# Kernel optimization log

Hardware: AMD Instinct MI355X
Metric: run time of the kernel (lower is better)

## Reference

```python
import jax, jax.numpy as jnp
import numpy as np
from jax import lax

EPS = 1e-5
WBITS, BBITS, ABITS = 8, 8, 11  # weight/bias/activation precisions (class defaults)


def _ste_round(x):
    # straight-through estimator round (matches HAWQ-style fake quant)
    return x + lax.stop_gradient(jnp.round(x) - x)


def _quant_weight(w, bits):
    # symmetric per-output-channel weight quantization
    n = 2.0 ** (bits - 1) - 1.0
    s = lax.stop_gradient(jnp.max(jnp.abs(w.reshape(w.shape[0], -1)), axis=1)) / n
    s = jnp.maximum(s, 1e-8)
    w_int = jnp.clip(_ste_round(w / s[:, None, None, None]), -n - 1.0, n)
    return w_int, s


def _conv(x, w, stride, pad):
    return lax.conv_general_dilated(
        x, w, (stride, stride), ((pad, pad), (pad, pad)),
        dimension_numbers=('NCHW', 'OIHW', 'NCHW'))


def _quant_bn_conv(x, act_scale, w, gamma, beta, mean, var, stride, pad):
    # fold BN into conv (QuantBnConv2d), quantize folded weight per channel,
    # integer conv in the x/act_scale domain, rescale back to float
    f = gamma * lax.rsqrt(var + EPS)
    w_f = w * f[:, None, None, None]
    b_f = beta - mean * f
    w_int, w_s = _quant_weight(w_f, WBITS)
    nb = 2.0 ** (BBITS - 1) - 1.0
    b_s = w_s * act_scale  # [O]
    b_int = jnp.clip(_ste_round(b_f / b_s), -nb - 1.0, nb)
    x_int = x / act_scale
    y_int = _conv(x_int, w_int, stride, pad) + b_int[None, :, None, None]
    return y_int * b_s[None, :, None, None], w_s


def _quant_conv(x, act_scale, w, stride, pad):
    # plain QuantConv2d (shortcut path, no bias)
    w_int, w_s = _quant_weight(w, WBITS)
    y_int = _conv(x / act_scale, w_int, stride, pad)
    scale = w_s * act_scale  # [O]
    return y_int * scale[None, :, None, None], w_s


def _quant_act(x, bits):
    # QuantAct: symmetric dynamic requantization to `bits` bits
    n = 2.0 ** (bits - 1) - 1.0
    s = jnp.maximum(lax.stop_gradient(jnp.max(jnp.abs(x))) / n, 1e-8)
    xq = jnp.clip(_ste_round(x / s), -n - 1.0, n) * s
    return xq, s


def setup_inputs() -> dict:
    key = jax.random.key(0)
    ks = jax.random.split(key, 12)
    B, Cin, Cout, H = 64, 128, 256, 56
    return {
        'x': jax.random.normal(ks[0], (B, Cin, H, H), jnp.float32),
        'act_scale': jnp.ones((1,), jnp.float32) * 0.05,
        'w_sc': jax.random.normal(ks[1], (Cout, Cin, 1, 1), jnp.float32) * 0.05,
        'w1': jax.random.normal(ks[2], (Cout, Cin, 3, 3), jnp.float32) * 0.05,
        'g1': jax.random.uniform(ks[3], (Cout,), jnp.float32) + 0.5,
        'b1': jax.random.normal(ks[4], (Cout,), jnp.float32) * 0.1,
        'm1': jax.random.normal(ks[5], (Cout,), jnp.float32) * 0.1,
        'v1': jax.random.uniform(ks[6], (Cout,), jnp.float32) + 0.5,
        'w2': jax.random.normal(ks[7], (Cout, Cout, 3, 3), jnp.float32) * 0.05,
        'g2': jax.random.uniform(ks[8], (Cout,), jnp.float32) + 0.5,
        'b2': jax.random.normal(ks[9], (Cout,), jnp.float32) * 0.1,
        'm2': jax.random.normal(ks[10], (Cout,), jnp.float32) * 0.1,
        'v2': jax.random.uniform(ks[11], (Cout,), jnp.float32) + 0.5,
    }


def reference(x, act_scale, w_sc, w1, g1, b1, m1, v1, w2, g2, b2, m2, v2):
    # resize_identity branch of QBlock.forward (stride-2 stage transition)
    short_x, _ = _quant_conv(x, act_scale, w_sc, stride=2, pad=0)
    out, _ = _quant_bn_conv(x, act_scale, w1, g1, b1, m1, v1, stride=2, pad=1)
    out = jax.nn.relu(out)
    out, a = _quant_act(out, ABITS)
    out, _ = _quant_bn_conv(out, a, w2, g2, b2, m2, v2, stride=1, pad=1)
    out = jax.nn.relu(out)
    out, a = _quant_act(out, ABITS)
    out = jax.nn.relu(out + short_x)
    out, a = _quant_act(out, ABITS)
    return out, a
```

## Files before the change

kernel.cpp:

```cpp
#include <hip/hip_runtime.h>
#include <cstdio>
#include <cstdint>

typedef _Float16 h8 __attribute__((ext_vector_type(8)));
typedef _Float16 h4 __attribute__((ext_vector_type(4)));
typedef _Float16 h2 __attribute__((ext_vector_type(2)));
typedef float f4 __attribute__((ext_vector_type(4)));

#define GLD16(g, l) __builtin_amdgcn_global_load_lds( \
    (const __attribute__((address_space(1))) void*)(g), \
    (__attribute__((address_space(3))) void*)(l), 16, 0, 0)

static constexpr int HOUT = 28;
static constexpr long long NSP = 64LL * HOUT * HOUT;
static constexpr long long NEL = NSP * 256;
static constexpr int NSLOT = 64;
static constexpr int SLOTSTRIDE = 32;

__global__ void init_ws(int* __restrict__ slots, _Float16* __restrict__ zp)
{
    const int t = threadIdx.x;
    for (int i = t; i < 3 * NSLOT * SLOTSTRIDE; i += 256) slots[i] = 0;
    for (int i = t; i < 512; i += 256) zp[i] = (_Float16)0.f;
}

__device__ __forceinline__ float slot_max(const int* __restrict__ slots)
{
    float m = 0.f;
#pragma unroll
    for (int i = 0; i < NSLOT; ++i) m = fmaxf(m, __int_as_float(slots[i * SLOTSTRIDE]));
    return m;
}

__global__ void prep_w1(const float* __restrict__ w1, const float* __restrict__ g1,
                        const float* __restrict__ b1, const float* __restrict__ m1,
                        const float* __restrict__ v1, const float* __restrict__ asp,
                        _Float16* __restrict__ wq, float* __restrict__ scale1,
                        float* __restrict__ bias1)
{
    const int o = blockIdx.x, t = threadIdx.x;
    const float f = g1[o] * rsqrtf(v1[o] + 1e-5f);
    const float* wr = w1 + (size_t)o * 1152;
    float amax = 0.f;
    for (int i = t; i < 1152; i += 256) amax = fmaxf(amax, fabsf(wr[i] * f));
    __shared__ float red[256];
    red[t] = amax; __syncthreads();
    for (int s = 128; s > 0; s >>= 1) { if (t < s) red[t] = fmaxf(red[t], red[t + s]); __syncthreads(); }
    const float ws = fmaxf(red[0] / 127.f, 1e-8f);
    for (int idx = t; idx < 2304; idx += 256) {
        int p = idx >> 8, cc = idx & 255, ci = cc & 127;
        float q = fminf(fmaxf(rintf(wr[ci * 9 + p] * f / ws), -128.f), 127.f);
        wq[(size_t)o * 2304 + idx] = (_Float16)q;
    }
    if (t == 0) {
        const float bs = ws * asp[0];
        const float bf = b1[o] - m1[o] * f;
        float bq = fminf(fmaxf(rintf(bf / bs), -128.f), 127.f);
        scale1[o] = bs;
        bias1[o] = bq * bs;
    }
}

__global__ void prep_w2(const float* __restrict__ w2, const float* __restrict__ g2,
                        const float* __restrict__ b2, const float* __restrict__ m2,
                        const float* __restrict__ v2,
                        _Float16* __restrict__ wq, float* __restrict__ ws2,
                        float* __restrict__ b2f)
{
    const int o = blockIdx.x, t = threadIdx.x;
    const float f = g2[o] * rsqrtf(v2[o] + 1e-5f);
    const float* wr = w2 + (size_t)o * 2304;
    float amax = 0.f;
    for (int i = t; i < 2304; i += 256) amax = fmaxf(amax, fabsf(wr[i] * f));
    __shared__ float red[256];
    red[t] = amax; __syncthreads();
    for (int s = 128; s > 0; s >>= 1) { if (t < s) red[t] = fmaxf(red[t], red[t + s]); __syncthreads(); }
    const float ws = fmaxf(red[0] / 127.f, 1e-8f);
    for (int idx = t; idx < 2304; idx += 256) {
        int p = idx >> 8, ci = idx & 255;
        float q = fminf(fmaxf(rintf(wr[ci * 9 + p] * f / ws), -128.f), 127.f);
        wq[(size_t)o * 2304 + idx] = (_Float16)q;
    }
    if (t == 0) { ws2[o] = ws; b2f[o] = b2[o] - m2[o] * f; }
}

__global__ void prep_wsc(const float* __restrict__ wsc, const float* __restrict__ asp,
                         _Float16* __restrict__ wq, float* __restrict__ scale_sc)
{
    const int o = blockIdx.x, t = threadIdx.x;
    const float* wr = wsc + (size_t)o * 128;
    float amax = (t < 128) ? fabsf(wr[t]) : 0.f;
    __shared__ float red[256];
    red[t] = amax; __syncthreads();
    for (int s = 128; s > 0; s >>= 1) { if (t < s) red[t] = fmaxf(red[t], red[t + s]); __syncthreads(); }
    const float ws = fmaxf(red[0] / 127.f, 1e-8f);
    float q = fminf(fmaxf(rintf(wr[t & 127] / ws), -128.f), 127.f);
    wq[(size_t)o * 256 + t] = (_Float16)q;
    if (t == 0) scale_sc[o] = ws * asp[0];
}

__global__ void prep_x(const float* __restrict__ x, const float* __restrict__ asp,
                       _Float16* __restrict__ xf)
{
    const int b = blockIdx.x / 56, h = blockIdx.x - (blockIdx.x / 56) * 56;
    const float as = asp[0];
    __shared__ float tile[56 * 129];
    const float* src = x + ((size_t)b * 128 * 56 + h) * 56;
    for (int i = threadIdx.x; i < 7168; i += 256) {
        int c = i / 56, ww = i - c * 56;
        tile[ww * 129 + c] = src[(size_t)c * 3136 + ww] / as;
    }
    __syncthreads();
    _Float16* dst = xf + (size_t)(b * 56 + h) * 2 * 28 * 256;
    for (int j = threadIdx.x; j < 7168; j += 256) {
        int ww = j >> 7, q = j & 127;
        int cc = q * 2;
        int c0 = cc & 127, c1 = (cc + 1) & 127;
        float x0 = tile[ww * 129 + c0];
        float x1 = tile[ww * 129 + c1];
        h2 o;
        if (cc < 128) { o[0] = (_Float16)x0; o[1] = (_Float16)x1; }
        else {
            _Float16 h0 = (_Float16)x0, h1 = (_Float16)x1;
            o[0] = (_Float16)(x0 - (float)h0);
            o[1] = (_Float16)(x1 - (float)h1);
        }
        size_t eo = ((size_t)(ww & 1) * 28 + (ww >> 1)) * 256 + (size_t)cc;
        *(h2*)&dst[eo] = o;
    }
}

template<int MODE>
__global__ __launch_bounds__(512, 1)
void conv_k(const _Float16* __restrict__ Xf,
            const _Float16* __restrict__ Wq,
            const _Float16* __restrict__ Wsc,
            const float* __restrict__ scale,
            const float* __restrict__ bias,
            const float* __restrict__ scale_sc,
            float* __restrict__ Y,
            float* __restrict__ Ysc,
            int* __restrict__ slots,
            const _Float16* __restrict__ zp)
{
    constexpr int KT = 2304;
    constexpr int NSTEP = 72;
    __shared__ __attribute__((aligned(16))) _Float16 L[49152];
    __shared__ float wred[8];

    const int t = threadIdx.x;
    const int wave = t >> 6, lane = t & 63;
    const int wm = wave >> 2;
    const int wn = wave & 3;
    const int fr = lane & 15, fq = lane >> 4;

    const int orig = blockIdx.x;
    const int xcd = orig & 7, i8 = orig >> 3;
    const int wgid = (xcd < 4 ? xcd * 25 : 100 + (xcd - 4) * 24) + i8;
    const int n0 = wgid << 8;

    const int srow = wn * 64 + lane;
    const char* aSrc = (const char*)Wq + (size_t)srow * (KT * 2);
    const int nb = n0 + srow;
    const int bb = nb / 784;
    const int rbp = nb - bb * 784;
    const int ohb = rbp / 28, owb = rbp - (rbp / 28) * 28;

    const char* bptr = (const char*)zp;
    auto stage = [&](int tt, int slot) {
        char* base = (char*)L + slot * 32768;
        if ((tt & 7) == 0) {
            const int p = tt >> 3;
            const int kh = p / 3, kw = p - kh * 3;
            if constexpr (MODE == 0) {
                int ih = ohb * 2 - 1 + kh;
                int par = (kw == 1) ? 0 : 1;
                int j = (kw == 0) ? owb - 1 : owb;
                bool ok = ((unsigned)ih < 56u) && ((unsigned)j < 28u);
                bptr = ok ? (const char*)Xf + (((((size_t)bb * 56 + ih) * 2 + par) * 28 + j) << 9)
                          : (const char*)zp;
            } else {
                int ih = ohb - 1 + kh, iw = owb - 1 + kw;
                bool ok = ((unsigned)ih < 28u) && ((unsigned)iw < 28u);
                bptr = ok ? (const char*)Xf + ((((size_t)bb * 28 + ih) * 28 + iw) << 9)
                          : (const char*)zp;
            }
        }
        const size_t ka = (size_t)tt * 64;
        const int ko = (tt & 7) * 64;
        GLD16(aSrc + ka + wm * 16,          base + wm * 4096 + wn * 1024);
        GLD16(aSrc + ka + (2 + wm) * 16,    base + (2 + wm) * 4096 + wn * 1024);
        GLD16(bptr + ko + wm * 16,          base + 16384 + wm * 4096 + wn * 1024);
        GLD16(bptr + ko + (2 + wm) * 16,    base + 16384 + (2 + wm) * 4096 + wn * 1024);
    };

    f4 acc[8][4];
#pragma unroll
    for (int i = 0; i < 8; ++i)
#pragma unroll
        for (int j = 0; j < 4; ++j) acc[i][j] = f4{0.f, 0.f, 0.f, 0.f};

    stage(0, 0);
    stage(1, 1);
    int cs = 0, ns = 2;
#pragma unroll 1
    for (int it = 0; it < NSTEP - 1; ++it) {
        asm volatile("s_waitcnt vmcnt(4)" ::: "memory");
        __builtin_amdgcn_s_barrier();
        const _Float16* Sa = &L[cs * 16384];
        const _Float16* Sb = Sa + 8192;
        h8 af0[4], af1[4], bf[4];
#pragma unroll
        for (int i = 0; i < 4; ++i) {
            af0[i] = *(const h8*)&Sa[fq * 2048 + (wm * 128 + i * 16 + fr) * 8];
            bf[i]  = *(const h8*)&Sb[fq * 2048 + (wn * 64 + i * 16 + fr) * 8];
        }
#pragma unroll
        for (int i = 0; i < 4; ++i)
            af1[i] = *(const h8*)&Sa[fq * 2048 + (wm * 128 + 64 + i * 16 + fr) * 8];
        if (it + 2 < NSTEP) stage(it + 2, ns);
        __builtin_amdgcn_s_setprio(1);
#pragma unroll
        for (int mi = 0; mi < 4; ++mi)
#pragma unroll
            for (int ni = 0; ni < 4; ++ni)
                acc[mi][ni] = __builtin_amdgcn_mfma_f32_16x16x32_f16(af0[mi], bf[ni], acc[mi][ni], 0, 0, 0);
#pragma unroll
        for (int mi = 0; mi < 4; ++mi)
#pragma unroll
            for (int ni = 0; ni < 4; ++ni)
                acc[4 + mi][ni] = __builtin_amdgcn_mfma_f32_16x16x32_f16(af1[mi], bf[ni], acc[4 + mi][ni], 0, 0, 0);
        __builtin_amdgcn_s_setprio(0);
        cs = (cs == 2) ? 0 : cs + 1;
        ns = (ns == 2) ? 0 : ns + 1;
    }
    {
        asm volatile("s_waitcnt vmcnt(0)" ::: "memory");
        __builtin_amdgcn_s_barrier();
        const _Float16* Sa = &L[cs * 16384];
        const _Float16* Sb = Sa + 8192;
        h8 af0[4], af1[4], bf[4];
#pragma unroll
        for (int i = 0; i < 4; ++i) {
            af0[i] = *(const h8*)&Sa[fq * 2048 + (wm * 128 + i * 16 + fr) * 8];
            bf[i]  = *(const h8*)&Sb[fq * 2048 + (wn * 64 + i * 16 + fr) * 8];
        }
#pragma unroll
        for (int i = 0; i < 4; ++i)
            af1[i] = *(const h8*)&Sa[fq * 2048 + (wm * 128 + 64 + i * 16 + fr) * 8];
#pragma unroll
        for (int mi = 0; mi < 4; ++mi)
#pragma unroll
            for (int ni = 0; ni < 4; ++ni)
                acc[mi][ni] = __builtin_amdgcn_mfma_f32_16x16x32_f16(af0[mi], bf[ni], acc[mi][ni], 0, 0, 0);
#pragma unroll
        for (int mi = 0; mi < 4; ++mi)
#pragma unroll
            for (int ni = 0; ni < 4; ++ni)
                acc[4 + mi][ni] = __builtin_amdgcn_mfma_f32_16x16x32_f16(af1[mi], bf[ni], acc[4 + mi][ni], 0, 0, 0);
    }

    float tmax = 0.f;
#pragma unroll
    for (int mi = 0; mi < 8; ++mi) {
        const int m = wm * 128 + mi * 16 + fq * 4;
        const f4 sc = *(const f4*)&scale[m];
        const f4 bi = *(const f4*)&bias[m];
#pragma unroll
        for (int ni = 0; ni < 4; ++ni) {
            const int n = n0 + wn * 64 + ni * 16 + fr;
            f4 v = acc[mi][ni] * sc + bi;
            f4 r;
            r.x = fmaxf(v.x, 0.f); r.y = fmaxf(v.y, 0.f);
            r.z = fmaxf(v.z, 0.f); r.w = fmaxf(v.w, 0.f);
            tmax = fmaxf(tmax, fmaxf(fmaxf(r.x, r.y), fmaxf(r.z, r.w)));
            *(f4*)&Y[(size_t)n * 256 + m] = r;
        }
    }
#pragma unroll
    for (int off = 32; off > 0; off >>= 1)
        tmax = fmaxf(tmax, __shfl_xor(tmax, off));
    if (lane == 0) wred[wave] = tmax;
    __syncthreads();
    if (t == 0) {
        float mx = 0.f;
#pragma unroll
        for (int i = 0; i < 8; ++i) mx = fmaxf(mx, wred[i]);
        atomicMax(&slots[(wgid & (NSLOT - 1)) * SLOTSTRIDE], __float_as_int(mx));
    }

    if constexpr (MODE == 0) {
        const char* pb[4];
#pragma unroll
        for (int ni = 0; ni < 4; ++ni) {
            int n = n0 + wn * 64 + ni * 16 + fr;
            int b2 = n / 784;
            int r2 = n - b2 * 784;
            int oh2 = r2 / 28, ow2 = r2 - (r2 / 28) * 28;
            pb[ni] = (const char*)Xf + (((((size_t)b2 * 56 + oh2 * 2) * 2 + 0) * 28 + ow2) << 9);
        }
#pragma unroll
        for (int i = 0; i < 8; ++i)
#pragma unroll
            for (int j = 0; j < 4; ++j) acc[i][j] = f4{0.f, 0.f, 0.f, 0.f};
#pragma unroll 1
        for (int st = 0; st < 8; ++st) {
            h8 sf[8], bg[4];
#pragma unroll
            for (int mi = 0; mi < 8; ++mi)
                sf[mi] = *(const h8*)((const char*)Wsc +
                         (size_t)(wm * 128 + mi * 16 + fr) * 512 + st * 64 + fq * 16);
#pragma unroll
            for (int ni = 0; ni < 4; ++ni)
                bg[ni] = *(const h8*)(pb[ni] + st * 64 + fq * 16);
#pragma unroll
            for (int mi = 0; mi < 8; ++mi)
#pragma unroll
                for (int ni = 0; ni < 4; ++ni)
                    acc[mi][ni] = __builtin_amdgcn_mfma_f32_16x16x32_f16(sf[mi], bg[ni], acc[mi][ni], 0, 0, 0);
        }
#pragma unroll
        for (int mi = 0; mi < 8; ++mi) {
            const int m = wm * 128 + mi * 16 + fq * 4;
            const f4 ssc = *(const f4*)&scale_sc[m];
#pragma unroll
            for (int ni = 0; ni < 4; ++ni) {
                const int n = n0 + wn * 64 + ni * 16 + fr;
                f4 s = acc[mi][ni] * ssc;
                *(f4*)&Ysc[(size_t)n * 256 + m] = s;
            }
        }
    }
}

__global__ void mid_k(const int* __restrict__ slotsA, const float* __restrict__ ws2,
                      const float* __restrict__ b2f, float* __restrict__ scale2,
                      float* __restrict__ bias2, float* __restrict__ a1p)
{
    const int o = threadIdx.x;
    const float a1 = fmaxf(slot_max(slotsA) / 1023.f, 1e-8f);
    const float s2 = ws2[o] * a1;
    float bq = fminf(fmaxf(rintf(b2f[o] / s2), -128.f), 127.f);
    scale2[o] = s2;
    bias2[o] = bq * s2;
    if (o == 0) a1p[0] = a1;
}

__global__ void quant_x2(const float* __restrict__ t1, const float* __restrict__ a1p,
                         _Float16* __restrict__ x2)
{
    const size_t i = (size_t)blockIdx.x * 256 + threadIdx.x;
    const float a1 = a1p[0];
    f4 v = ((const f4*)t1)[i];
    h4 o;
    o[0] = (_Float16)fminf(rintf(v.x / a1), 1023.f);
    o[1] = (_Float16)fminf(rintf(v.y / a1), 1023.f);
    o[2] = (_Float16)fminf(rintf(v.z / a1), 1023.f);
    o[3] = (_Float16)fminf(rintf(v.w / a1), 1023.f);
    ((h4*)x2)[i] = o;
}

__global__ void add_short_k(const float* __restrict__ t2, const float* __restrict__ sh,
                            const int* __restrict__ slotsB, int* __restrict__ slotsC,
                            float* __restrict__ o3)
{
    const float a2 = fmaxf(slot_max(slotsB) / 1023.f, 1e-8f);
    const float inv_a2 = 1.f / a2;
    float tmax = 0.f;
    const size_t base = (size_t)blockIdx.x * 256 + threadIdx.x;
#pragma unroll
    for (int it = 0; it < 4; ++it) {
        const size_t i = base + (size_t)it * 802816;
        f4 v = ((const f4*)t2)[i];
        f4 s = ((const f4*)sh)[i];
        f4 r;
        r.x = fmaxf(fminf(rintf(v.x * inv_a2), 1023.f) * a2 + s.x, 0.f);
        r.y = fmaxf(fminf(rintf(v.y * inv_a2), 1023.f) * a2 + s.y, 0.f);
        r.z = fmaxf(fminf(rintf(v.z * inv_a2), 1023.f) * a2 + s.z, 0.f);
        r.w = fmaxf(fminf(rintf(v.w * inv_a2), 1023.f) * a2 + s.w, 0.f);
        ((f4*)o3)[i] = r;
        tmax = fmaxf(tmax, fmaxf(fmaxf(r.x, r.y), fmaxf(r.z, r.w)));
    }
#pragma unroll
    for (int off = 32; off > 0; off >>= 1)
        tmax = fmaxf(tmax, __shfl_xor(tmax, off));
    __shared__ float wred[4];
    if ((threadIdx.x & 63) == 0) wred[threadIdx.x >> 6] = tmax;
    __syncthreads();
    if (threadIdx.x == 0) {
        float mx = fmaxf(fmaxf(wred[0], wred[1]), fmaxf(wred[2], wred[3]));
        atomicMax(&slotsC[(blockIdx.x & (NSLOT - 1)) * SLOTSTRIDE], __float_as_int(mx));
    }
}

__global__ void finalize_k(const float* __restrict__ o3, const int* __restrict__ slotsC,
                           float* __restrict__ dout, int out_size)
{
    const int b = blockIdx.x / 28, oh = blockIdx.x - (blockIdx.x / 28) * 28;
    const float a3 = fmaxf(slot_max(slotsC) / 1023.f, 1e-8f);
    __shared__ float tile[28 * 257];
    const float* src = o3 + (size_t)(b * 28 + oh) * 28 * 256;
    for (int i = threadIdx.x; i < 7168; i += 256)
        tile[(i >> 8) * 257 + (i & 255)] = src[i];
    __syncthreads();
    for (int j = threadIdx.x; j < 7168; j += 256) {
        int c = j / 28, ww = j - (j / 28) * 28;
        float v = tile[ww * 257 + c];
        float q = fminf(rintf(v / a3), 1023.f);
        dout[(((size_t)b * 256 + c) * 28 + oh) * 28 + ww] = q * a3;
    }
    if (blockIdx.x == 0 && threadIdx.x == 0) dout[(size_t)out_size - 1] = a3;
}

extern "C" void kernel_launch(void* const* d_in, const int* in_sizes, int n_in,
                              void* d_out, int out_size, void* d_ws, size_t ws_size,
                              hipStream_t stream)
{
    const float* x   = (const float*)d_in[0];
    const float* as_ = (const float*)d_in[1];
    const float* wsc = (const float*)d_in[2];
    const float* w1  = (const float*)d_in[3];
    const float* g1  = (const float*)d_in[4];
    const float* b1  = (const float*)d_in[5];
    const float* m1  = (const float*)d_in[6];
    const float* v1  = (const float*)d_in[7];
    const float* w2  = (const float*)d_in[8];
    const float* g2  = (const float*)d_in[9];
    const float* b2  = (const float*)d_in[10];
    const float* m2  = (const float*)d_in[11];
    const float* v2  = (const float*)d_in[12];
    float* out = (float*)d_out;

    char* w = (char*)d_ws;
    size_t off = 0;
    auto alloc = [&](size_t bytes) { size_t c = off; off += (bytes + 255) & ~(size_t)255; return c; };
    const size_t oXF = alloc((size_t)64 * 56 * 56 * 256 * 2);
    const size_t oY1 = alloc((size_t)NEL * 4);
    const size_t oSH = alloc((size_t)NEL * 4);
    const size_t oX2 = alloc((size_t)NEL * 2);
    const size_t oW1 = alloc((size_t)256 * 2304 * 2);
    const size_t oW2 = alloc((size_t)256 * 2304 * 2);
    const size_t oWS = alloc((size_t)256 * 256 * 2);
    const size_t oSC = alloc((size_t)8 * 256 * 4);
    const size_t oMS = alloc(3 * NSLOT * SLOTSTRIDE * 4 + 2048);
    if (off > ws_size) {
        fprintf(stderr, "kernel_launch: ws too small: need %zu have %zu\n", off, ws_size);
        return;
    }

    _Float16* xf   = (_Float16*)(w + oXF);
    float*    y1   = (float*)(w + oY1);
    float*    sh   = (float*)(w + oSH);
    _Float16* x2   = (_Float16*)(w + oX2);
    _Float16* wq1  = (_Float16*)(w + oW1);
    _Float16* wq2  = (_Float16*)(w + oW2);
    _Float16* wscd = (_Float16*)(w + oWS);
    float* scl = (float*)(w + oSC);
    float *scale1 = scl, *bias1 = scl + 256, *scale_sc = scl + 512, *ws2 = scl + 768,
          *b2f = scl + 1024, *scale2 = scl + 1280, *bias2 = scl + 1536, *a1p = scl + 1792;
    int* slots  = (int*)(w + oMS);
    int* slotsA = slots;
    int* slotsB = slots + NSLOT * SLOTSTRIDE;
    int* slotsC = slots + 2 * NSLOT * SLOTSTRIDE;
    _Float16* zp = (_Float16*)(w + oMS + 3 * NSLOT * SLOTSTRIDE * 4);
    float* y2 = (float*)(w + oXF);
    float* o3 = (float*)(w + oY1);

    init_ws<<<1, 256, 0, stream>>>(slots, zp);
    prep_wsc<<<256, 256, 0, stream>>>(wsc, as_, wscd, scale_sc);
    prep_w1<<<256, 256, 0, stream>>>(w1, g1, b1, m1, v1, as_, wq1, scale1, bias1);
    prep_w2<<<256, 256, 0, stream>>>(w2, g2, b2, m2, v2, wq2, ws2, b2f);
    prep_x<<<64 * 56, 256, 0, stream>>>(x, as_, xf);
    conv_k<0><<<196, 512, 0, stream>>>(xf, wq1, wscd, scale1, bias1, scale_sc,
                                       y1, sh, slotsA, zp);
    mid_k<<<1, 256, 0, stream>>>(slotsA, ws2, b2f, scale2, bias2, a1p);
    quant_x2<<<12544, 256, 0, stream>>>(y1, a1p, x2);
    conv_k<1><<<196, 512, 0, stream>>>(x2, wq2, nullptr, scale2, bias2, nullptr,
                                       y2, nullptr, slotsB, zp);
    add_short_k<<<3136, 256, 0, stream>>>(y2, sh, slotsB, slotsC, o3);
    finalize_k<<<64 * 28, 256, 0, stream>>>(o3, slotsC, out, out_size);
}
```

Measured before the change: 366.4 us.

## Deepen conv main-loop pipeline to four LDS stages with split half-phases

Restructures the conv GEMM main loop from a 3-slot LDS ring to a 4-slot ring with a prefetch distance of 3 K-steps. Each K-step is split into two halves: each half issues half of the next stage's global-to-LDS loads, then runs 16 MFMAs, with barriers, lgkmcnt waits and sched_barriers between the halves. This is meant to keep more global loads in flight and interleave loads with MFMA work to hide memory latency. In exchange it uses more LDS (128KB), adds more barriers per iteration, and waits on vmcnt counts that depend on how many K-steps remain.

```diff
diff --git a/kernel.cpp b/kernel.cpp
--- a/kernel.cpp
+++ b/kernel.cpp
@@ -143,127 +143,118 @@
             int* __restrict__ slots,
             const _Float16* __restrict__ zp)
 {
-    constexpr int KT = 2304;
-    constexpr int NSTEP = 72;
-    __shared__ __attribute__((aligned(16))) _Float16 L[49152];
+    constexpr int NH = 72;
+    __shared__ __attribute__((aligned(16))) _Float16 L[65536];
     __shared__ float wred[8];
 
     const int t = threadIdx.x;
-    const int wave = t >> 6, lane = t & 63;
-    const int wm = wave >> 2;
-    const int wn = wave & 3;
-    const int fr = lane & 15, fq = lane >> 4;
+    const int w = t >> 6, lane = t & 63;
+    const int wm = w >> 2, wn = w & 3;
+    const int fr = lane & 15, fqr = lane >> 4;
 
     const int orig = blockIdx.x;
     const int xcd = orig & 7, i8 = orig >> 3;
     const int wgid = (xcd < 4 ? xcd * 25 : 100 + (xcd - 4) * 24) + i8;
     const int n0 = wgid << 8;
 
-    const int srow = wn * 64 + lane;
-    const char* aSrc = (const char*)Wq + (size_t)srow * (KT * 2);
+    const int srow = (w & 3) * 64 + lane;
+    const char* aSrc = (const char*)Wq + (size_t)srow * 4608;
     const int nb = n0 + srow;
     const int bb = nb / 784;
     const int rbp = nb - bb * 784;
     const int ohb = rbp / 28, owb = rbp - (rbp / 28) * 28;
+    const int fqs = w >> 2;
+    const int dgr = w * 64;
 
     const char* bptr = (const char*)zp;
-    auto stage = [&](int tt, int slot) {
-        char* base = (char*)L + slot * 32768;
-        if ((tt & 7) == 0) {
-            const int p = tt >> 3;
-            const int kh = p / 3, kw = p - kh * 3;
-            if constexpr (MODE == 0) {
-                int ih = ohb * 2 - 1 + kh;
-                int par = (kw == 1) ? 0 : 1;
-                int j = (kw == 0) ? owb - 1 : owb;
-                bool ok = ((unsigned)ih < 56u) && ((unsigned)j < 28u);
-                bptr = ok ? (const char*)Xf + (((((size_t)bb * 56 + ih) * 2 + par) * 28 + j) << 9)
-                          : (const char*)zp;
-            } else {
-                int ih = ohb - 1 + kh, iw = owb - 1 + kw;
-                bool ok = ((unsigned)ih < 28u) && ((unsigned)iw < 28u);
-                bptr = ok ? (const char*)Xf + ((((size_t)bb * 28 + ih) * 28 + iw) << 9)
-                          : (const char*)zp;
-            }
-        }
-        const size_t ka = (size_t)tt * 64;
-        const int ko = (tt & 7) * 64;
-        GLD16(aSrc + ka + wm * 16,          base + wm * 4096 + wn * 1024);
-        GLD16(aSrc + ka + (2 + wm) * 16,    base + (2 + wm) * 4096 + wn * 1024);
-        GLD16(bptr + ko + wm * 16,          base + 16384 + wm * 4096 + wn * 1024);
-        GLD16(bptr + ko + (2 + wm) * 16,    base + 16384 + (2 + wm) * 4096 + wn * 1024);
+    auto set_tap = [&](int kt) {
+        const int p = kt >> 3;
+        const int kh = p / 3, kw = p - kh * 3;
+        if constexpr (MODE == 0) {
+            int ih = ohb * 2 - 1 + kh;
+            int par = (kw == 1) ? 0 : 1;
+            int j = (kw == 0) ? owb - 1 : owb;
+            bool ok = ((unsigned)ih < 56u) && ((unsigned)j < 28u);
+            bptr = ok ? (const char*)Xf + (((((size_t)bb * 56 + ih) * 2 + par) * 28 + j) << 9)
+                      : (const char*)zp;
+        } else {
+            int ih = ohb - 1 + kh, iw = owb - 1 + kw;
+            bool ok = ((unsigned)ih < 28u) && ((unsigned)iw < 28u);
+            bptr = ok ? (const char*)Xf + ((((size_t)bb * 28 + ih) * 28 + iw) << 9)
+                      : (const char*)zp;
+        }
     };
 
+    auto stage_part = [&](int kt, int j) {
+        if (kt >= NH) return;
+        char* base = (char*)L + (size_t)(kt & 3) * 32768;
+        const int fq = 2 * j + fqs;
+        if (j == 0 && (kt & 7) == 0) set_tap(kt);
+        GLD16(aSrc + (size_t)kt * 64 + fq * 16, base + (j * 512 + dgr) * 16);
+        GLD16(bptr + (kt & 7) * 64 + fq * 16,   base + 16384 + (j * 512 + dgr) * 16);
+    };
+
     f4 acc[8][4];
 #pragma unroll
     for (int i = 0; i < 8; ++i)
 #pragma unroll
         for (int j = 0; j < 4; ++j) acc[i][j] = f4{0.f, 0.f, 0.f, 0.f};
 
-    stage(0, 0);
-    stage(1, 1);
-    int cs = 0, ns = 2;
+    stage_part(0, 0); stage_part(0, 1);
+    stage_part(1, 0); stage_part(1, 1);
+    stage_part(2, 0); stage_part(2, 1);
+    asm volatile("s_waitcnt vmcnt(8)" ::: "memory");
+    __builtin_amdgcn_s_barrier();
+
 #pragma unroll 1
-    for (int it = 0; it < NSTEP - 1; ++it) {
-        asm volatile("s_waitcnt vmcnt(4)" ::: "memory");
+    for (int kt = 0; kt < NH; ++kt) {
+        const char* SA = (const char*)L + (size_t)(kt & 3) * 32768;
+        const char* SB = SA + 16384;
+        h8 af0[4], bf[4];
+#pragma unroll
+        for (int i = 0; i < 4; ++i) {
+            af0[i] = *(const h8*)(SA + fqr * 4096 + (wm * 128 + i * 16 + fr) * 16);
+            bf[i]  = *(const h8*)(SB + fqr * 4096 + (wn * 64 + i * 16 + fr) * 16);
+        }
+        stage_part(kt + 3, 0);
         __builtin_amdgcn_s_barrier();
-        const _Float16* Sa = &L[cs * 16384];
-        const _Float16* Sb = Sa + 8192;
-        h8 af0[4], af1[4], bf[4];
-#pragma unroll
-        for (int i = 0; i < 4; ++i) {
-            af0[i] = *(const h8*)&Sa[fq * 2048 + (wm * 128 + i * 16 + fr) * 8];
-            bf[i]  = *(const h8*)&Sb[fq * 2048 + (wn * 64 + i * 16 + fr) * 8];
-        }
-#pragma unroll
-        for (int i = 0; i < 4; ++i)
-            af1[i] = *(const h8*)&Sa[fq * 2048 + (wm * 128 + 64 + i * 16 + fr) * 8];
-        if (it + 2 < NSTEP) stage(it + 2, ns);
+        asm volatile("s_waitcnt lgkmcnt(0)" ::: "memory");
+        __builtin_amdgcn_sched_barrier(0);
         __builtin_amdgcn_s_setprio(1);
 #pragma unroll
         for (int mi = 0; mi < 4; ++mi)
 #pragma unroll
             for (int ni = 0; ni < 4; ++ni)
                 acc[mi][ni] = __builtin_amdgcn_mfma_f32_16x16x32_f16(af0[mi], bf[ni], acc[mi][ni], 0, 0, 0);
+        __builtin_amdgcn_s_setprio(0);
+        __builtin_amdgcn_s_barrier();
+
+        h8 af1[4];
+#pragma unroll
+        for (int i = 0; i < 4; ++i)
+            af1[i] = *(const h8*)(SA + fqr * 4096 + (wm * 128 + 64 + i * 16 + fr) * 16);
+        stage_part(kt + 3, 1);
+        __builtin_amdgcn_s_barrier();
+        asm volatile("s_waitcnt lgkmcnt(0)" ::: "memory");
+        __builtin_amdgcn_sched_barrier(0);
+        __builtin_amdgcn_s_setprio(1);
 #pragma unroll
         for (int mi = 0; mi < 4; ++mi)
 #pragma unroll
             for (int ni = 0; ni < 4; ++ni)
                 acc[4 + mi][ni] = __builtin_amdgcn_mfma_f32_16x16x32_f16(af1[mi], bf[ni], acc[4 + mi][ni], 0, 0, 0);
         __builtin_amdgcn_s_setprio(0);
-        cs = (cs == 2) ? 0 : cs + 1;
-        ns = (ns == 2) ? 0 : ns + 1;
-    }
-    {
-        asm volatile("s_waitcnt vmcnt(0)" ::: "memory");
+        const int rem = (NH - 2) - kt;
+        if (rem >= 2)      { asm volatile("s_waitcnt vmcnt(8)" ::: "memory"); }
+        else if (rem == 1) { asm volatile("s_waitcnt vmcnt(4)" ::: "memory"); }
+        else if (rem == 0) { asm volatile("s_waitcnt vmcnt(0)" ::: "memory"); }
         __builtin_amdgcn_s_barrier();
-        const _Float16* Sa = &L[cs * 16384];
-        const _Float16* Sb = Sa + 8192;
-        h8 af0[4], af1[4], bf[4];
-#pragma unroll
-        for (int i = 0; i < 4; ++i) {
-            af0[i] = *(const h8*)&Sa[fq * 2048 + (wm * 128 + i * 16 + fr) * 8];
-            bf[i]  = *(const h8*)&Sb[fq * 2048 + (wn * 64 + i * 16 + fr) * 8];
-        }
-#pragma unroll
-        for (int i = 0; i < 4; ++i)
-            af1[i] = *(const h8*)&Sa[fq * 2048 + (wm * 128 + 64 + i * 16 + fr) * 8];
-#pragma unroll
-        for (int mi = 0; mi < 4; ++mi)
-#pragma unroll
-            for (int ni = 0; ni < 4; ++ni)
-                acc[mi][ni] = __builtin_amdgcn_mfma_f32_16x16x32_f16(af0[mi], bf[ni], acc[mi][ni], 0, 0, 0);
-#pragma unroll
-        for (int mi = 0; mi < 4; ++mi)
-#pragma unroll
-            for (int ni = 0; ni < 4; ++ni)
-                acc[4 + mi][ni] = __builtin_amdgcn_mfma_f32_16x16x32_f16(af1[mi], bf[ni], acc[4 + mi][ni], 0, 0, 0);
     }
 
     float tmax = 0.f;
 #pragma unroll
     for (int mi = 0; mi < 8; ++mi) {
-        const int m = wm * 128 + mi * 16 + fq * 4;
+        const int m = wm * 128 + mi * 16 + fqr * 4;
         const f4 sc = *(const f4*)&scale[m];
         const f4 bi = *(const f4*)&bias[m];
 #pragma unroll
@@ -280,7 +271,7 @@
 #pragma unroll
     for (int off = 32; off > 0; off >>= 1)
         tmax = fmaxf(tmax, __shfl_xor(tmax, off));
-    if (lane == 0) wred[wave] = tmax;
+    if (lane == 0) wred[w] = tmax;
     __syncthreads();
     if (t == 0) {
         float mx = 0.f;
@@ -309,10 +300,10 @@
 #pragma unroll
             for (int mi = 0; mi < 8; ++mi)
                 sf[mi] = *(const h8*)((const char*)Wsc +
-                         (size_t)(wm * 128 + mi * 16 + fr) * 512 + st * 64 + fq * 16);
+                         (size_t)(wm * 128 + mi * 16 + fr) * 512 + st * 64 + fqr * 16);
 #pragma unroll
             for (int ni = 0; ni < 4; ++ni)
-                bg[ni] = *(const h8*)(pb[ni] + st * 64 + fq * 16);
+                bg[ni] = *(const h8*)(pb[ni] + st * 64 + fqr * 16);
 #pragma unroll
             for (int mi = 0; mi < 8; ++mi)
 #pragma unroll
@@ -321,7 +312,7 @@
         }
 #pragma unroll
         for (int mi = 0; mi < 8; ++mi) {
-            const int m = wm * 128 + mi * 16 + fq * 4;
+            const int m = wm * 128 + mi * 16 + fqr * 4;
             const f4 ssc = *(const f4*)&scale_sc[m];
 #pragma unroll
             for (int ni = 0; ni < 4; ++ni) {
```

Measured after the change: 437.7 us. 19.4% more time.
